# Kernel optimization log

Measured on AMD Instinct MI355X. Metric: run time of the kernel, lower is better.

The kernel has to match this reference:

```python
import jax, jax.numpy as jnp
import numpy as np

H = 1024       # hidden_size
R = 4          # downsacale_ratio -> bottleneck H//R = 256
DI = 2048      # mamba d_inner = expand * H
NS = 16        # d_state
KC = 4         # d_conv
DTR = 64       # dt_rank = ceil(H/16)
B, L = 4, 1024


def setup_inputs() -> dict:
    key = jax.random.key(0)
    ks = iter(jax.random.split(key, 32))
    w = lambda shape, s=0.02: jax.random.normal(next(ks), shape, jnp.float32) * s
    Hr = H // R
    inp = {
        'x': jax.random.normal(next(ks), (B, L, H), jnp.float32),
        't': jax.random.normal(next(ks), (B, H), jnp.float32),
        # adaLN modulation: SiLU -> Linear(H, 3H)
        'ada_w': w((H, 3 * H)), 'ada_b': jnp.zeros((3 * H,), jnp.float32),
        # hg_dense: Linear(H,H/R) SiLU Linear(H/R,H)
        'hgd_w1': w((H, Hr)), 'hgd_b1': jnp.zeros((Hr,), jnp.float32),
        'hgd_w2': w((Hr, H)), 'hgd_b2': jnp.zeros((H,), jnp.float32),
        # Mamba params
        'in_proj_w': w((H, 2 * DI)),
        'conv_w': w((DI, KC), 0.1), 'conv_b': jnp.zeros((DI,), jnp.float32),
        'x_proj_w': w((DI, DTR + 2 * NS)),
        'dt_proj_w': w((DTR, DI), 0.1),
        'dt_proj_b': jnp.log(jnp.expm1(jnp.full((DI,), 0.01, jnp.float32))),  # softplus^-1(0.01)
        'A_log': jnp.log(jnp.broadcast_to(jnp.arange(1, NS + 1, dtype=jnp.float32), (DI, NS))),
        'Dp': jnp.ones((DI,), jnp.float32),
        'out_proj_w': w((DI, H)),
        # hg_fuse
        'fm_w': w((H, Hr)), 'fm_b': jnp.zeros((Hr,), jnp.float32),
        'fr_w': w((H, Hr)), 'fr_b': jnp.zeros((Hr,), jnp.float32),
        'ff_w': w((Hr, H)), 'ff_b': jnp.zeros((H,), jnp.float32),
    }
    return inp


def _ln(x, eps=1e-6):
    mu = jnp.mean(x, -1, keepdims=True)
    var = jnp.mean(jnp.square(x - mu), -1, keepdims=True)
    return (x - mu) / jnp.sqrt(var + eps)


def _mamba(xd, in_proj_w, conv_w, conv_b, x_proj_w, dt_proj_w, dt_proj_b, A_log, Dp, out_proj_w):
    # xd: [B, L, H]
    xz = xd @ in_proj_w                      # [B, L, 2*DI]
    xm, z = jnp.split(xz, 2, axis=-1)
    # causal depthwise conv over time
    xc = jnp.swapaxes(xm, 1, 2)              # [B, DI, L]
    xc = jax.lax.conv_general_dilated(
        xc, conv_w[:, None, :], window_strides=(1,), padding=[(KC - 1, 0)],
        feature_group_count=DI, dimension_numbers=('NCH', 'OIH', 'NCH'))
    xc = jax.nn.silu(jnp.swapaxes(xc, 1, 2) + conv_b)   # [B, L, DI]
    dbl = xc @ x_proj_w                      # [B, L, DTR + 2*NS]
    dt = jax.nn.softplus(dbl[..., :DTR] @ dt_proj_w + dt_proj_b)   # [B, L, DI]
    Bm = dbl[..., DTR:DTR + NS]              # [B, L, NS]
    Cm = dbl[..., DTR + NS:]                 # [B, L, NS]
    A = -jnp.exp(A_log)                      # [DI, NS]

    def step(h, inp):
        dt_t, x_t, B_t, C_t = inp            # [B,DI],[B,DI],[B,NS],[B,NS]
        dA = jnp.exp(dt_t[:, :, None] * A)                       # [B, DI, NS]
        h = dA * h + (dt_t * x_t)[:, :, None] * B_t[:, None, :]
        y = jnp.einsum('bdn,bn->bd', h, C_t)
        return h, y

    h0 = jnp.zeros((xd.shape[0], DI, NS), xd.dtype)
    seq = (jnp.moveaxis(dt, 1, 0), jnp.moveaxis(xc, 1, 0),
           jnp.moveaxis(Bm, 1, 0), jnp.moveaxis(Cm, 1, 0))
    _, ys = jax.lax.scan(step, h0, seq)
    y = jnp.moveaxis(ys, 0, 1) + xc * Dp     # [B, L, DI]
    y = y * jax.nn.silu(z)
    return y @ out_proj_w                    # [B, L, H]


def reference(x, t, ada_w, ada_b, hgd_w1, hgd_b1, hgd_w2, hgd_b2,
              in_proj_w, conv_w, conv_b, x_proj_w, dt_proj_w, dt_proj_b,
              A_log, Dp, out_proj_w, fm_w, fm_b, fr_w, fr_b, ff_w, ff_b):
    ada = jax.nn.silu(t) @ ada_w + ada_b               # [B, 3H]
    shift, scale, alpha = jnp.split(ada, 3, axis=-1)
    x1 = _ln(x) * (1 + scale[:, None, :]) + shift[:, None, :]
    xd = jax.nn.silu(x1 @ hgd_w1 + hgd_b1) @ hgd_w2 + hgd_b2
    x1_2 = _mamba(xd, in_proj_w, conv_w, conv_b, x_proj_w, dt_proj_w,
                  dt_proj_b, A_log, Dp, out_proj_w)
    a = jax.nn.silu(x1_2 @ fm_w + fm_b)
    b = jax.nn.silu(x1 @ fr_w + fr_b)
    fuse = (a * b) @ ff_w + ff_b
    return x + alpha[:, None, :] * fuse
```

## Files before the change

### kernel.cpp

```cpp
#include <hip/hip_runtime.h>
#include <math.h>
#include <stdint.h>

#define H_   1024
#define HR_  256
#define DI_  2048
#define NS_  16
#define KC_  4
#define DTR_ 64
#define B_   4
#define L_   1024
#define ROWS (B_*L_)
#define H3_  3072
#define NCH_ 32
#define CL_  32
#define CLT_ 8

typedef short bf16x8 __attribute__((ext_vector_type(8)));
typedef float f32x4  __attribute__((ext_vector_type(4)));

#if __has_builtin(__builtin_amdgcn_exp2f)
#define EXP2(x) __builtin_amdgcn_exp2f(x)
#else
#define EXP2(x) __expf((x) * 0.6931471805599453f)
#endif
#define LOG2E 1.4426950408889634f

__device__ __forceinline__ float silu_f(float v) { return v / (1.f + __expf(-v)); }

__device__ __forceinline__ uint32_t pack_bf16_2(float a, float b) {
    uint32_t ua = __float_as_uint(a);
    uint32_t ub = __float_as_uint(b);
    uint32_t ra = (ua + 0x7FFFu + ((ua >> 16) & 1u)) >> 16;
    uint32_t rb = (ub + 0x7FFFu + ((ub >> 16) & 1u)) >> 16;
    return ra | (rb << 16);
}
__device__ __forceinline__ unsigned short cvt_bf16(float a) {
    uint32_t ua = __float_as_uint(a);
    return (unsigned short)((ua + 0x7FFFu + ((ua >> 16) & 1u)) >> 16);
}
__device__ __forceinline__ float bf16_to_f(unsigned short u) {
    return __uint_as_float(((uint32_t)u) << 16);
}

__device__ __forceinline__ void gload16(const short* g, short* l) {
    __builtin_amdgcn_global_load_lds(
        (const __attribute__((address_space(1))) void*)g,
        (__attribute__((address_space(3))) void*)l, 16, 0, 0);
}

#define TW_HGDFR 0ull
#define TW_HGD2  524288ull
#define TW_INPJ  786432ull
#define TW_XPJ   4980736ull
#define TW_DTPJ  5242880ull
#define TW_OPJ   5373952ull
#define TW_FM    7471104ull
#define TW_FF    7733248ull
#define TWT      7995392ull

__global__ __launch_bounds__(256) void wtrans_kernel(
    const float* __restrict__ s0, const float* __restrict__ s1,
    const float* __restrict__ s2, const float* __restrict__ s3,
    const float* __restrict__ s4, const float* __restrict__ s5,
    const float* __restrict__ s6, const float* __restrict__ s7,
    const float* __restrict__ s8, short* __restrict__ wt)
{
    int bid = blockIdx.x;
    const float* src; short* dst; int K, N, rel;
    if      (bid < 256)  { src = s0; dst = wt + TW_HGDFR;          K = 1024; N = 256;  rel = bid; }
    else if (bid < 512)  { src = s1; dst = wt + TW_HGDFR + 262144; K = 1024; N = 256;  rel = bid - 256; }
    else if (bid < 768)  { src = s2; dst = wt + TW_HGD2;           K = 256;  N = 1024; rel = bid - 512; }
    else if (bid < 4864) { src = s3; dst = wt + TW_INPJ;           K = 1024; N = 4096; rel = bid - 768; }
    else if (bid < 5120) { src = s4; dst = wt + TW_XPJ;            K = 2048; N = 96;   rel = bid - 4864; }
    else if (bid < 5248) { src = s5; dst = wt + TW_DTPJ;           K = 64;   N = 2048; rel = bid - 5120; }
    else if (bid < 7296) { src = s6; dst = wt + TW_OPJ;            K = 2048; N = 1024; rel = bid - 5248; }
    else if (bid < 7552) { src = s7; dst = wt + TW_FM;             K = 1024; N = 256;  rel = bid - 7296; }
    else                 { src = s8; dst = wt + TW_FF;             K = 256;  N = 1024; rel = bid - 7552; }
    int tkc = K >> 5;
    int tk = rel % tkc, tn = rel / tkc;

    __shared__ float ld[32][33];
    int tx = threadIdx.x & 7, ty = threadIdx.x >> 3;
    int kk = tk * 32 + ty, nn = tn * 32 + tx * 4;
    float4 v = make_float4(0.f, 0.f, 0.f, 0.f);
    if (nn < N) v = *(const float4*)&src[(size_t)kk * N + nn];
    ld[ty][tx * 4 + 0] = v.x; ld[ty][tx * 4 + 1] = v.y;
    ld[ty][tx * 4 + 2] = v.z; ld[ty][tx * 4 + 3] = v.w;
    __syncthreads();
    int nn2 = tn * 32 + ty, kk2 = tk * 32 + tx * 4;
    float a0 = ld[tx * 4 + 0][ty], a1 = ld[tx * 4 + 1][ty];
    float a2 = ld[tx * 4 + 2][ty], a3 = ld[tx * 4 + 3][ty];
    uint2 p = { pack_bf16_2(a0, a1), pack_bf16_2(a2, a3) };
    *(uint2*)&dst[(size_t)nn2 * K + kk2] = p;
}

__global__ __launch_bounds__(256) void cwt_kernel(
    const float* __restrict__ conv_w, float* __restrict__ cwt)
{
    int d = blockIdx.x * 256 + threadIdx.x;
    float4 v = *(const float4*)&conv_w[d * KC_];
    cwt[0 * DI_ + d] = v.x;
    cwt[1 * DI_ + d] = v.y;
    cwt[2 * DI_ + d] = v.z;
    cwt[3 * DI_ + d] = v.w;
}

__global__ __launch_bounds__(256) void ada_part_kernel(
    const float* __restrict__ t, const float* __restrict__ ada_w,
    float* __restrict__ part)
{
    int col = blockIdx.x * 1024 + threadIdx.x * 4;
    int b = blockIdx.y, z = blockIdx.z;
    __shared__ float st[32];
    if (threadIdx.x < 32) {
        float v = t[b * H_ + z * 32 + threadIdx.x];
        st[threadIdx.x] = silu_f(v);
    }
    __syncthreads();
    float4 acc = make_float4(0.f, 0.f, 0.f, 0.f);
    const float* w = ada_w + (size_t)(z * 32) * H3_ + col;
    #pragma unroll
    for (int k = 0; k < 32; ++k) {
        float4 wv = *(const float4*)(w + (size_t)k * H3_);
        float s = st[k];
        acc.x = fmaf(s, wv.x, acc.x);
        acc.y = fmaf(s, wv.y, acc.y);
        acc.z = fmaf(s, wv.z, acc.z);
        acc.w = fmaf(s, wv.w, acc.w);
    }
    *(float4*)&part[((size_t)z * B_ + b) * H3_ + col] = acc;
}

__global__ __launch_bounds__(256) void ada_red_kernel(
    const float* __restrict__ part, const float* __restrict__ ada_b,
    float* __restrict__ ada)
{
    int i = (blockIdx.x * 256 + threadIdx.x) * 4;
    int b = i / H3_, col = i - b * H3_;
    float4 s = make_float4(0.f, 0.f, 0.f, 0.f);
    #pragma unroll
    for (int z = 0; z < 32; ++z) {
        float4 p = *(const float4*)&part[((size_t)z * B_ + b) * H3_ + col];
        s.x += p.x; s.y += p.y; s.z += p.z; s.w += p.w;
    }
    float4 bv = *(const float4*)&ada_b[col];
    s.x += bv.x; s.y += bv.y; s.z += bv.z; s.w += bv.w;
    *(float4*)&ada[(size_t)b * H3_ + col] = s;
}

__global__ __launch_bounds__(256) void ln_mod_kernel(
    const float* __restrict__ x, const float* __restrict__ ada,
    short* __restrict__ x1b)
{
    int row = blockIdx.x;
    int b   = row >> 10;
    const float* xr = x + (size_t)row * H_;
    float4 v = ((const float4*)xr)[threadIdx.x];
    float s  = v.x + v.y + v.z + v.w;
    float s2 = v.x*v.x + v.y*v.y + v.z*v.z + v.w*v.w;

    __shared__ float red[8];
    int wave = threadIdx.x >> 6, lane = threadIdx.x & 63;
    #pragma unroll
    for (int off = 32; off; off >>= 1) {
        s  += __shfl_down(s,  off);
        s2 += __shfl_down(s2, off);
    }
    if (lane == 0) { red[wave] = s; red[4 + wave] = s2; }
    __syncthreads();
    float ts  = red[0] + red[1] + red[2] + red[3];
    float ts2 = red[4] + red[5] + red[6] + red[7];
    float mu  = ts  * (1.f / H_);
    float var = ts2 * (1.f / H_) - mu * mu;
    float inv = rsqrtf(var + 1e-6f);

    const float* sh = ada + b * H3_;
    int i = threadIdx.x * 4;
    float4 sh4 = *(const float4*)&sh[i];
    float4 sc4 = *(const float4*)&sh[H_ + i];
    float ox = (v.x - mu) * inv * (1.f + sc4.x) + sh4.x;
    float oy = (v.y - mu) * inv * (1.f + sc4.y) + sh4.y;
    float oz = (v.z - mu) * inv * (1.f + sc4.z) + sh4.z;
    float ow = (v.w - mu) * inv * (1.f + sc4.w) + sh4.w;
    uint2 p = { pack_bf16_2(ox, oy), pack_bf16_2(oz, ow) };
    *(uint2*)(x1b + (size_t)row * H_ + i) = p;
}

template<int ACT, bool SPLITK>
__global__ __launch_bounds__(256) void gemm128(
    const short* __restrict__ A, int lda,
    const short* __restrict__ Wt, int ldw,
    const float* __restrict__ bias,
    float* __restrict__ C, short* __restrict__ Cb, short* __restrict__ Cb2,
    int ldc, int M, int N, int K,
    const float* __restrict__ E0, const float* __restrict__ E1)
{
    __shared__ short As[3][4096];
    __shared__ short Bs[3][4096];
    int tid  = threadIdx.x;
    int lane = tid & 63, wv = tid >> 6, wm = wv >> 1, wn = wv & 1;
    int n0 = blockIdx.x * 128;
    int m0 = blockIdx.y * 128;

    if (SPLITK) {
        int z = blockIdx.z;
        A  += (size_t)z * K;
        Wt += (size_t)z * K;
        C  += (size_t)z * M * N;
    }

    int r = lane & 15, g = lane >> 4;
    int sA = wv * 2;
    const short* ga0 = A  + (size_t)(m0 + sA * 16 + r) * lda + g * 8;
    const short* ga1 = ga0 + (size_t)16 * lda;
    const short* gb0 = Wt + (size_t)(n0 + sA * 16 + r) * ldw + g * 8;
    const short* gb1 = gb0 + (size_t)16 * ldw;

    f32x4 acc[4][4];
    #pragma unroll
    for (int i = 0; i < 4; ++i)
        #pragma unroll
        for (int j = 0; j < 4; ++j) {
            acc[i][j][0] = 0.f; acc[i][j][1] = 0.f;
            acc[i][j][2] = 0.f; acc[i][j][3] = 0.f;
        }

    #define STAGE(buf, koff)                                    \
        do {                                                    \
            gload16(ga0 + (koff), &As[buf][sA * 512]);          \
            gload16(ga1 + (koff), &As[buf][sA * 512 + 512]);    \
            gload16(gb0 + (koff), &Bs[buf][sA * 512]);          \
            gload16(gb1 + (koff), &Bs[buf][sA * 512 + 512]);    \
        } while (0)

    #define COMPUTE(buf)                                                          \
        do {                                                                      \
            bf16x8 af[4], bfr[4];                                                 \
            _Pragma("unroll")                                                     \
            for (int i = 0; i < 4; ++i)                                           \
                af[i] = *(const bf16x8*)&As[buf][(wm * 4 + i) * 512 + lane * 8];  \
            _Pragma("unroll")                                                     \
            for (int j = 0; j < 4; ++j)                                           \
                bfr[j] = *(const bf16x8*)&Bs[buf][(wn * 4 + j) * 512 + lane * 8]; \
            _Pragma("unroll")                                                     \
            for (int i = 0; i < 4; ++i)                                           \
                _Pragma("unroll")                                                 \
                for (int j = 0; j < 4; ++j)                                       \
                    acc[i][j] = __builtin_amdgcn_mfma_f32_16x16x32_bf16(          \
                        af[i], bfr[j], acc[i][j], 0, 0, 0);                       \
        } while (0)

    int T = K >> 5;
    STAGE(0, 0);
    if (T > 1) STAGE(1, 32);
    for (int t = 0; t < T; ++t) {
        if (t + 1 < T) asm volatile("s_waitcnt vmcnt(4)" ::: "memory");
        else           asm volatile("s_waitcnt vmcnt(0)" ::: "memory");
        __builtin_amdgcn_s_barrier();
        if (t + 2 < T) STAGE((t + 2) % 3, (t + 2) * 32);
        COMPUTE(t % 3);
    }
    #undef STAGE
    #undef COMPUTE

    #pragma unroll
    for (int i = 0; i < 4; ++i) {
        int mb = m0 + wm * 64 + i * 16 + ((lane >> 4) << 2);
        #pragma unroll
        for (int j = 0; j < 4; ++j) {
            int n = n0 + wn * 64 + j * 16 + (lane & 15);
            if (n < N) {
                float bv;
                if (ACT == 6) bv = (n < 256) ? bias[n] : E0[n - 256];
                else          bv = bias ? bias[n] : 0.f;
                #pragma unroll
                for (int rr = 0; rr < 4; ++rr) {
                    int m = mb + rr;
                    float v = acc[i][j][rr] + bv;
                    size_t ci = (size_t)m * ldc + n;
                    if (ACT == 6) {
                        float sv = silu_f(v);
                        if (n < 256) Cb[(size_t)m * 256 + n]        = (short)cvt_bf16(sv);
                        else         Cb2[(size_t)m * 256 + (n-256)] = (short)cvt_bf16(sv);
                    } else {
                        if (ACT == 2) v = (v > 20.f) ? v : log1pf(__expf(v));
                        else if (ACT == 4) {
                            int bb = m >> 10;
                            v = E0[ci] + E1[bb * H3_ + 2 * H_ + n] * v;
                        }
                        if (C)  C[ci]  = v;
                        if (Cb) Cb[ci] = (short)cvt_bf16(v);
                    }
                }
            }
        }
    }
}

template<int ACT>
__global__ __launch_bounds__(512) void gemm256(
    const short* __restrict__ A, int lda,
    const short* __restrict__ Wt, int ldw,
    short* __restrict__ Cb, int M, int N, int K)
{
    extern __shared__ short lds[];
    short* Asb = lds;
    short* Bsb = lds + 24576;
    int tid  = threadIdx.x;
    int lane = tid & 63, wv = tid >> 6;
    int wm = wv >> 2, wn = wv & 3;
    int n0 = blockIdx.x * 256;
    int m0 = blockIdx.y * 256;

    int r = lane & 15, g = lane >> 4;
    int sA = wv * 2;
    const short* ga0 = A  + (size_t)(m0 + sA * 16 + r) * lda + g * 8;
    const short* ga1 = ga0 + (size_t)16 * lda;
    const short* gb0 = Wt + (size_t)(n0 + sA * 16 + r) * ldw + g * 8;
    const short* gb1 = gb0 + (size_t)16 * ldw;

    f32x4 acc[8][4];
    #pragma unroll
    for (int i = 0; i < 8; ++i)
        #pragma unroll
        for (int j = 0; j < 4; ++j) {
            acc[i][j][0] = 0.f; acc[i][j][1] = 0.f;
            acc[i][j][2] = 0.f; acc[i][j][3] = 0.f;
        }

    #define STAGE2(buf, koff)                                       \
        do {                                                        \
            gload16(ga0 + (koff), &Asb[(buf) * 8192 + sA * 512]);   \
            gload16(ga1 + (koff), &Asb[(buf) * 8192 + sA * 512 + 512]); \
            gload16(gb0 + (koff), &Bsb[(buf) * 8192 + sA * 512]);   \
            gload16(gb1 + (koff), &Bsb[(buf) * 8192 + sA * 512 + 512]); \
        } while (0)

    int T = K >> 5;
    STAGE2(0, 0);
    if (T > 1) STAGE2(1, 32);
    for (int t = 0; t < T; ++t) {
        if (t + 1 < T) asm volatile("s_waitcnt vmcnt(4)" ::: "memory");
        else           asm volatile("s_waitcnt vmcnt(0)" ::: "memory");
        __builtin_amdgcn_s_barrier();
        if (t + 2 < T) STAGE2((t + 2) % 3, (t + 2) * 32);
        {
            int buf = t % 3;
            bf16x8 af[8], bfr[4];
            #pragma unroll
            for (int i = 0; i < 8; ++i)
                af[i] = *(const bf16x8*)&Asb[buf * 8192 + (wm * 8 + i) * 512 + lane * 8];
            #pragma unroll
            for (int j = 0; j < 4; ++j)
                bfr[j] = *(const bf16x8*)&Bsb[buf * 8192 + (wn * 4 + j) * 512 + lane * 8];
            __builtin_amdgcn_s_setprio(1);
            #pragma unroll
            for (int i = 0; i < 8; ++i)
                #pragma unroll
                for (int j = 0; j < 4; ++j)
                    acc[i][j] = __builtin_amdgcn_mfma_f32_16x16x32_bf16(
                        af[i], bfr[j], acc[i][j], 0, 0, 0);
            __builtin_amdgcn_s_setprio(0);
        }
    }
    #undef STAGE2

    #pragma unroll
    for (int i = 0; i < 8; ++i) {
        int mb = m0 + wm * 128 + i * 16 + ((lane >> 4) << 2);
        #pragma unroll
        for (int j = 0; j < 4; ++j) {
            int n = n0 + wn * 64 + j * 16 + (lane & 15);
            #pragma unroll
            for (int rr = 0; rr < 4; ++rr) {
                int m = mb + rr;
                float v = acc[i][j][rr];
                if (ACT == 5) {
                    size_t idx = (n < DI_) ? ((size_t)m * DI_ + n)
                                           : ((size_t)ROWS * DI_ + (size_t)m * DI_ + (n - DI_));
                    Cb[idx] = (short)cvt_bf16(v);
                }
            }
        }
    }
}

template<int ACT, bool SPLITK>
__global__ __launch_bounds__(512) void gemm256d(
    const short* __restrict__ A, int lda,
    const short* __restrict__ Wt, int ldw,
    short* __restrict__ Cb, int ldc,
    int M, int N, int K)
{
    extern __shared__ short lds[];
    short* Asb = lds;
    short* Bsb = lds + 16384;
    int tid  = threadIdx.x;
    int lane = tid & 63, wv = tid >> 6;
    int wm = wv >> 2, wn = wv & 3;
    int n0 = blockIdx.x * 256;
    int m0 = blockIdx.y * 256;

    if (SPLITK) {
        int z = blockIdx.z;
        A  += (size_t)z * K;
        Wt += (size_t)z * K;
        Cb += (size_t)z * M * N;
    }

    int r = lane & 15, g = lane >> 4;
    int sA = wv * 2;
    const short* ga0 = A  + (size_t)(m0 + sA * 16 + r) * lda + g * 8;
    const short* ga1 = ga0 + (size_t)16 * lda;
    const short* gb0 = Wt + (size_t)(n0 + sA * 16 + r) * ldw + g * 8;
    const short* gb1 = gb0 + (size_t)16 * ldw;

    f32x4 acc[8][4];
    #pragma unroll
    for (int i = 0; i < 8; ++i)
        #pragma unroll
        for (int j = 0; j < 4; ++j) {
            acc[i][j][0] = 0.f; acc[i][j][1] = 0.f;
            acc[i][j][2] = 0.f; acc[i][j][3] = 0.f;
        }

    #define STAGE2(buf, koff)                                       \
        do {                                                        \
            gload16(ga0 + (koff), &Asb[(buf) * 8192 + sA * 512]);   \
            gload16(ga1 + (koff), &Asb[(buf) * 8192 + sA * 512 + 512]); \
            gload16(gb0 + (koff), &Bsb[(buf) * 8192 + sA * 512]);   \
            gload16(gb1 + (koff), &Bsb[(buf) * 8192 + sA * 512 + 512]); \
        } while (0)

    int T = K >> 5;
    STAGE2(0, 0);
    __syncthreads();
    int cur = 0;
    for (int t = 0; t < T; ++t) {
        if (t + 1 < T) STAGE2(cur ^ 1, (t + 1) * 32);
        {
            bf16x8 af[8], bfr[4];
            #pragma unroll
            for (int i = 0; i < 8; ++i)
                af[i] = *(const bf16x8*)&Asb[cur * 8192 + (wm * 8 + i) * 512 + lane * 8];
            #pragma unroll
            for (int j = 0; j < 4; ++j)
                bfr[j] = *(const bf16x8*)&Bsb[cur * 8192 + (wn * 4 + j) * 512 + lane * 8];
            __builtin_amdgcn_s_setprio(1);
            #pragma unroll
            for (int i = 0; i < 8; ++i)
                #pragma unroll
                for (int j = 0; j < 4; ++j)
                    acc[i][j] = __builtin_amdgcn_mfma_f32_16x16x32_bf16(
                        af[i], bfr[j], acc[i][j], 0, 0, 0);
            __builtin_amdgcn_s_setprio(0);
        }
        __syncthreads();
        cur ^= 1;
    }
    #undef STAGE2

    #pragma unroll
    for (int i = 0; i < 8; ++i) {
        int mb = m0 + wm * 128 + i * 16 + ((lane >> 4) << 2);
        #pragma unroll
        for (int j = 0; j < 4; ++j) {
            int n = n0 + wn * 64 + j * 16 + (lane & 15);
            #pragma unroll
            for (int rr = 0; rr < 4; ++rr) {
                int m = mb + rr;
                float v = acc[i][j][rr];
                if (ACT == 8) {
                    Cb[(size_t)m * ldc + n] = (short)cvt_bf16(v);
                }
            }
        }
    }
}

__global__ __launch_bounds__(256) void redk_xproj(
    const float* __restrict__ part, float* __restrict__ dbl,
    short* __restrict__ dblb)
{
    size_t i = ((size_t)blockIdx.x * 256 + threadIdx.x) * 4;
    const size_t seg = (size_t)ROWS * 96;
    float4 s = *(const float4*)(part + i);
    #pragma unroll
    for (int z = 1; z < 8; ++z) {
        float4 p = *(const float4*)(part + z * seg + i);
        s.x += p.x; s.y += p.y; s.z += p.z; s.w += p.w;
    }
    *(float4*)(dbl + i) = s;
    uint2 p = { pack_bf16_2(s.x, s.y), pack_bf16_2(s.z, s.w) };
    *(uint2*)(dblb + i) = p;
}

__global__ __launch_bounds__(256) void redk_hgdfr(
    const float* __restrict__ part, const float* __restrict__ hgd_b1,
    const float* __restrict__ fr_b, short* __restrict__ h1b,
    short* __restrict__ frlin)
{
    size_t i = ((size_t)blockIdx.x * 256 + threadIdx.x) * 4;
    const size_t seg = (size_t)ROWS * 512;
    int m   = (int)(i >> 9);
    int col = (int)(i & 511);
    float4 a = *(const float4*)(part + i);
    float4 b = *(const float4*)(part + seg + i);
    float s0 = a.x + b.x, s1 = a.y + b.y, s2 = a.z + b.z, s3 = a.w + b.w;
    const float* bias = (col < 256) ? (hgd_b1 + col) : (fr_b + col - 256);
    float4 bv = *(const float4*)bias;
    float o0 = silu_f(s0 + bv.x), o1 = silu_f(s1 + bv.y);
    float o2 = silu_f(s2 + bv.z), o3 = silu_f(s3 + bv.w);
    uint2 p = { pack_bf16_2(o0, o1), pack_bf16_2(o2, o3) };
    short* dst = (col < 256) ? (h1b + (size_t)m * 256 + col)
                             : (frlin + (size_t)m * 256 + col - 256);
    *(uint2*)dst = p;
}

__global__ __launch_bounds__(256) void redk_op4(
    const short* __restrict__ part, short* __restrict__ x12b)
{
    size_t i = ((size_t)blockIdx.x * 256 + threadIdx.x) * 8;
    const size_t seg = (size_t)ROWS * H_;
    float s[8];
    bf16x8 p0 = *(const bf16x8*)(part + i);
    #pragma unroll
    for (int e = 0; e < 8; ++e) s[e] = bf16_to_f((unsigned short)p0[e]);
    #pragma unroll
    for (int z = 1; z < 4; ++z) {
        bf16x8 pz = *(const bf16x8*)(part + z * seg + i);
        #pragma unroll
        for (int e = 0; e < 8; ++e) s[e] += bf16_to_f((unsigned short)pz[e]);
    }
    bf16x8 o;
    #pragma unroll
    for (int e = 0; e < 8; ++e) o[e] = (short)cvt_bf16(s[e]);
    *(bf16x8*)(x12b + i) = o;
}

__global__ __launch_bounds__(256) void redk_fm(
    const float* __restrict__ part, const float* __restrict__ fm_b,
    const short* __restrict__ frlin, short* __restrict__ abb)
{
    size_t i = ((size_t)blockIdx.x * 256 + threadIdx.x) * 4;
    const size_t seg = (size_t)ROWS * HR_;
    float4 s = *(const float4*)(part + i);
    #pragma unroll
    for (int z = 1; z < 4; ++z) {
        float4 p = *(const float4*)(part + z * seg + i);
        s.x += p.x; s.y += p.y; s.z += p.z; s.w += p.w;
    }
    int col = (int)(i & (HR_ - 1));
    float4 b = *(const float4*)(fm_b + col);
    const short* fr = frlin + i;
    float o0 = silu_f(s.x + b.x) * bf16_to_f((unsigned short)fr[0]);
    float o1 = silu_f(s.y + b.y) * bf16_to_f((unsigned short)fr[1]);
    float o2 = silu_f(s.z + b.z) * bf16_to_f((unsigned short)fr[2]);
    float o3 = silu_f(s.w + b.w) * bf16_to_f((unsigned short)fr[3]);
    uint2 p = { pack_bf16_2(o0, o1), pack_bf16_2(o2, o3) };
    *(uint2*)(abb + i) = p;
}

__global__ __launch_bounds__(256) void conv_kernel(
    const short* __restrict__ xmb, const float* __restrict__ cwt,
    const float* __restrict__ conv_b, short* __restrict__ xcb)
{
    int d0 = threadIdx.x * 8;
    int b  = blockIdx.y;
    int l0 = blockIdx.x * CLT_;

    float w[KC_][8];
    #pragma unroll
    for (int j = 0; j < KC_; ++j) {
        float4 a = *(const float4*)&cwt[j * DI_ + d0];
        float4 c = *(const float4*)&cwt[j * DI_ + d0 + 4];
        w[j][0] = a.x; w[j][1] = a.y; w[j][2] = a.z; w[j][3] = a.w;
        w[j][4] = c.x; w[j][5] = c.y; w[j][6] = c.z; w[j][7] = c.w;
    }
    float bia[8];
    {
        float4 b0 = *(const float4*)&conv_b[d0];
        float4 b1 = *(const float4*)&conv_b[d0 + 4];
        bia[0] = b0.x; bia[1] = b0.y; bia[2] = b0.z; bia[3] = b0.w;
        bia[4] = b1.x; bia[5] = b1.y; bia[6] = b1.z; bia[7] = b1.w;
    }

    const short* base = xmb + (size_t)b * L_ * DI_ + d0;
    short*       outb = xcb + (size_t)b * L_ * DI_ + d0;

    bf16x8 win[KC_];
    #pragma unroll
    for (int j = 0; j < KC_ - 1; ++j) {
        int ll = l0 - (KC_ - 1) + j;
        if (ll >= 0) win[j] = *(const bf16x8*)(base + (size_t)ll * DI_);
        else         win[j] = (bf16x8)0;
    }
    for (int l = l0; l < l0 + CLT_; ++l) {
        win[KC_ - 1] = *(const bf16x8*)(base + (size_t)l * DI_);
        bf16x8 o;
        #pragma unroll
        for (int e = 0; e < 8; ++e) {
            float acc = bia[e];
            #pragma unroll
            for (int j = 0; j < KC_; ++j)
                acc = fmaf(bf16_to_f((unsigned short)win[j][e]), w[j][e], acc);
            o[e] = (short)cvt_bf16(silu_f(acc));
        }
        *(bf16x8*)(outb + (size_t)l * DI_) = o;
        win[0] = win[1]; win[1] = win[2]; win[2] = win[3];
    }
}

__global__ __launch_bounds__(256) void scan_part1(
    const short* __restrict__ dtb, const short* __restrict__ xcb,
    const float* __restrict__ dbl, const float* __restrict__ A_log,
    float* __restrict__ hend, float* __restrict__ dtsum)
{
    int bx = blockIdx.x;
    int dg = bx & 15;
    int bc = bx >> 4;
    int c  = bc & (NCH_ - 1);
    int b  = bc >> 5;
    int tid  = threadIdx.x;
    int lane = tid & 63, wv = tid >> 6;
    int dl   = tid >> 1;
    int d    = dg * 128 + dl;
    int half = tid & 1;
    int n0   = half * 8;

    __shared__ float sB[CL_][NS_];
    __shared__ short dtS[2][16][128];
    __shared__ short xcS[2][16][128];

    size_t srcoff = (size_t)(b * L_ + c * CL_ + wv * 4 + (lane >> 4)) * DI_
                    + dg * 128 + (lane & 15) * 8;
    const short* gdt = dtb + srcoff;
    const short* gxc = xcb + srcoff;

    #define SSTG1(buf, q)                                             \
        do {                                                          \
            gload16(gdt + (size_t)(q) * 16 * DI_, &dtS[buf][wv*4][0]); \
            gload16(gxc + (size_t)(q) * 16 * DI_, &xcS[buf][wv*4][0]); \
        } while (0)

    SSTG1(0, 0);
    for (int idx = tid; idx < CL_ * NS_; idx += 256) {
        int l = idx >> 4, n = idx & 15;
        sB[l][n] = dbl[(size_t)(b * L_ + c * CL_ + l) * 96 + DTR_ + n];
    }
    float Aa2[8];
    #pragma unroll
    for (int n = 0; n < 8; ++n)
        Aa2[n] = -__expf(A_log[d * NS_ + n0 + n]) * LOG2E;

    float h[8];
    #pragma unroll
    for (int n = 0; n < 8; ++n) h[n] = 0.f;
    float sdt = 0.f;

    __syncthreads();
    int buf = 0;
    for (int q = 0; q < 2; ++q) {
        if (q < 1) SSTG1(buf ^ 1, q + 1);
        #pragma unroll
        for (int li = 0; li < 16; ++li) {
            int l = q * 16 + li;
            float dtv = bf16_to_f((unsigned short)dtS[buf][li][dl]);
            float xv  = bf16_to_f((unsigned short)xcS[buf][li][dl]);
            float du  = dtv * xv;
            sdt += dtv;
            #pragma unroll
            for (int n = 0; n < 8; ++n)
                h[n] = fmaf(EXP2(dtv * Aa2[n]), h[n], du * sB[l][n0 + n]);
        }
        __syncthreads();
        buf ^= 1;
    }
    #undef SSTG1

    #pragma unroll
    for (int n = 0; n < 8; ++n)
        hend[((size_t)((b * NCH_ + c) * NS_ + n0 + n)) * DI_ + d] = h[n];
    if (half == 0)
        dtsum[(size_t)(b * NCH_ + c) * DI_ + d] = sdt;
}

__global__ __launch_bounds__(256) void scan_mid(
    const float* __restrict__ hend, const float* __restrict__ dtsum,
    const float* __restrict__ A_log, float* __restrict__ hin)
{
    int idx = blockIdx.x * 256 + threadIdx.x;
    int d  = idx & (DI_ - 1);
    int bn = idx >> 11;
    int n  = bn & (NS_ - 1);
    int b  = bn >> 4;
    float Aa2 = -__expf(A_log[d * NS_ + n]) * LOG2E;
    float h = 0.f;
    #pragma unroll
    for (int c = 0; c < NCH_; ++c) {
        size_t o = ((size_t)((b * NCH_ + c) * NS_ + n)) * DI_ + d;
        hin[o] = h;
        float s = dtsum[(size_t)(b * NCH_ + c) * DI_ + d];
        h = fmaf(EXP2(Aa2 * s), h, hend[o]);
    }
}

__global__ __launch_bounds__(256) void scan_part2(
    const short* __restrict__ dtb, const short* __restrict__ xcb,
    const short* __restrict__ zb, const float* __restrict__ dbl,
    const float* __restrict__ A_log, const float* __restrict__ Dp,
    const float* __restrict__ hin, short* __restrict__ y2b)
{
    int bx = blockIdx.x;
    int dg = bx & 15;
    int bc = bx >> 4;
    int c  = bc & (NCH_ - 1);
    int b  = bc >> 5;
    int tid  = threadIdx.x;
    int lane = tid & 63, wv = tid >> 6;
    int dl   = tid >> 1;
    int d    = dg * 128 + dl;
    int half = tid & 1;
    int n0   = half * 8;

    __shared__ float sBC[CL_][2 * NS_];
    __shared__ short dtS[2][16][128];
    __shared__ short xcS[2][16][128];
    __shared__ short zS[2][16][128];

    size_t srcoff = (size_t)(b * L_ + c * CL_ + wv * 4 + (lane >> 4)) * DI_
                    + dg * 128 + (lane & 15) * 8;
    const short* gdt = dtb + srcoff;
    const short* gxc = xcb + srcoff;
    const short* gz  = zb  + srcoff;

    #define SSTG2(buf, q)                                             \
        do {                                                          \
            gload16(gdt + (size_t)(q) * 16 * DI_, &dtS[buf][wv*4][0]); \
            gload16(gxc + (size_t)(q) * 16 * DI_, &xcS[buf][wv*4][0]); \
            gload16(gz  + (size_t)(q) * 16 * DI_, &zS[buf][wv*4][0]);  \
        } while (0)

    SSTG2(0, 0);
    for (int idx = tid; idx < CL_ * 2 * NS_; idx += 256) {
        int l = idx >> 5, n = idx & 31;
        sBC[l][n] = dbl[(size_t)(b * L_ + c * CL_ + l) * 96 + DTR_ + n];
    }
    float Aa2[8];
    #pragma unroll
    for (int n = 0; n < 8; ++n)
        Aa2[n] = -__expf(A_log[d * NS_ + n0 + n]) * LOG2E;

    float h[8];
    #pragma unroll
    for (int n = 0; n < 8; ++n)
        h[n] = hin[((size_t)((b * NCH_ + c) * NS_ + n0 + n)) * DI_ + d];
    float Dpv = Dp[d];
    size_t obase = (size_t)(b * L_ + c * CL_) * DI_ + d;

    __syncthreads();
    int buf = 0;
    for (int q = 0; q < 2; ++q) {
        if (q < 1) SSTG2(buf ^ 1, q + 1);
        #pragma unroll
        for (int li = 0; li < 16; ++li) {
            int l = q * 16 + li;
            float dtv = bf16_to_f((unsigned short)dtS[buf][li][dl]);
            float xv  = bf16_to_f((unsigned short)xcS[buf][li][dl]);
            float zv  = bf16_to_f((unsigned short)zS[buf][li][dl]);
            float du  = dtv * xv;
            float y = 0.f;
            #pragma unroll
            for (int n = 0; n < 8; ++n) {
                float dA = EXP2(dtv * Aa2[n]);
                h[n] = fmaf(dA, h[n], du * sBC[l][n0 + n]);
                y = fmaf(h[n], sBC[l][NS_ + n0 + n], y);
            }
            y += __shfl_xor(y, 1);
            if (half == 0) {
                y = fmaf(xv, Dpv, y);
                y2b[obase + (size_t)l * DI_] = (short)cvt_bf16(y * silu_f(zv));
            }
        }
        __syncthreads();
        buf ^= 1;
    }
    #undef SSTG2
}

extern "C" void kernel_launch(void* const* d_in, const int* in_sizes, int n_in,
                              void* d_out, int out_size, void* d_ws, size_t ws_size,
                              hipStream_t stream)
{
    const float* x         = (const float*)d_in[0];
    const float* t         = (const float*)d_in[1];
    const float* ada_w     = (const float*)d_in[2];
    const float* ada_b     = (const float*)d_in[3];
    const float* hgd_w1    = (const float*)d_in[4];
    const float* hgd_b1    = (const float*)d_in[5];
    const float* hgd_w2    = (const float*)d_in[6];
    const float* hgd_b2    = (const float*)d_in[7];
    const float* in_proj_w = (const float*)d_in[8];
    const float* conv_w    = (const float*)d_in[9];
    const float* conv_b    = (const float*)d_in[10];
    const float* x_proj_w  = (const float*)d_in[11];
    const float* dt_proj_w = (const float*)d_in[12];
    const float* dt_proj_b = (const float*)d_in[13];
    const float* A_log     = (const float*)d_in[14];
    const float* Dp        = (const float*)d_in[15];
    const float* out_proj_w= (const float*)d_in[16];
    const float* fm_w      = (const float*)d_in[17];
    const float* fm_b      = (const float*)d_in[18];
    const float* fr_w      = (const float*)d_in[19];
    const float* fr_b      = (const float*)d_in[20];
    const float* ff_w      = (const float*)d_in[21];
    const float* ff_b      = (const float*)d_in[22];
    float* out = (float*)d_out;

    char* p = (char*)d_ws;
    auto alloc = [&](size_t bytes) { char* r = p; p += (bytes + 255) & ~255ull; return r; };

    short* wt      = (short*)alloc(TWT * 2);
    float* cwt     = (float*)alloc((size_t)KC_ * DI_ * 4);
    short* x1b     = (short*)alloc((size_t)ROWS * H_ * 2);
    short* h1b     = (short*)alloc((size_t)ROWS * HR_ * 2);
    short* frlin   = (short*)alloc((size_t)ROWS * HR_ * 2);
    short* xdb     = (short*)alloc((size_t)ROWS * H_ * 2);
    short* xmzb    = (short*)alloc((size_t)ROWS * DI_ * 4);
    short* xcb     = (short*)alloc((size_t)ROWS * DI_ * 2);
    short* y2b     = (short*)alloc((size_t)ROWS * DI_ * 2);
    short* dtb     = (short*)alloc((size_t)ROWS * DI_ * 2);
    float* scratch = (float*)alloc((size_t)4 * ROWS * H_ * 4);
    float* dbl     = (float*)alloc((size_t)ROWS * 96 * 4);
    short* dblb    = (short*)alloc((size_t)ROWS * 96 * 2);
    short* x12b    = (short*)alloc((size_t)ROWS * H_ * 2);
    short* abb     = (short*)alloc((size_t)ROWS * HR_ * 2);
    float* ada     = (float*)alloc((size_t)B_ * H3_ * 4);

    short* xmb   = xmzb;
    short* zb    = xmzb + (size_t)ROWS * DI_;
    float* dtsum = (float*)abb;
    float* adapart = scratch;
    float* hfpart  = scratch;
    float* xppart  = scratch;
    float* hend    = scratch;
    float* hin     = scratch + (size_t)B_ * NCH_ * NS_ * DI_;
    short* oppart  = (short*)scratch;
    float* fmpart  = scratch;

    dim3 blk(256), b512(512);

    wtrans_kernel<<<dim3(7808), blk, 0, stream>>>(
        hgd_w1, fr_w, hgd_w2, in_proj_w, x_proj_w, dt_proj_w, out_proj_w,
        fm_w, ff_w, wt);
    cwt_kernel<<<dim3(DI_ / 256), blk, 0, stream>>>(conv_w, cwt);
    ada_part_kernel<<<dim3(3, B_, 32), blk, 0, stream>>>(t, ada_w, adapart);
    ada_red_kernel<<<dim3(B_ * H3_ / 4 / 256), blk, 0, stream>>>(adapart, ada_b, ada);
    ln_mod_kernel<<<dim3(ROWS), blk, 0, stream>>>(x, ada, x1b);
    gemm128<0, true><<<dim3(4, 32, 2), blk, 0, stream>>>(
        x1b, H_, wt + TW_HGDFR, H_, nullptr, hfpart, nullptr, nullptr,
        512, ROWS, 512, 512, nullptr, nullptr);
    redk_hgdfr<<<dim3(ROWS * 512 / 4 / 256), blk, 0, stream>>>(
        hfpart, hgd_b1, fr_b, h1b, frlin);
    gemm128<0, false><<<dim3(8, 32), blk, 0, stream>>>(
        h1b, HR_, wt + TW_HGD2, HR_, hgd_b2, nullptr, xdb, nullptr,
        H_, ROWS, H_, HR_, nullptr, nullptr);
    gemm256<5><<<dim3(16, 16), b512, 98304, stream>>>(
        xdb, H_, wt + TW_INPJ, H_, xmb, ROWS, 2 * DI_, H_);
    conv_kernel<<<dim3(L_ / CLT_, B_), blk, 0, stream>>>(xmb, cwt, conv_b, xcb);
    gemm128<0, true><<<dim3(1, 32, 8), blk, 0, stream>>>(
        xcb, DI_, wt + TW_XPJ, DI_, nullptr, xppart, nullptr, nullptr,
        96, ROWS, 96, 256, nullptr, nullptr);
    redk_xproj<<<dim3(ROWS * 96 / 4 / 256), blk, 0, stream>>>(xppart, dbl, dblb);
    gemm128<2, false><<<dim3(16, 32), blk, 0, stream>>>(
        dblb, 96, wt + TW_DTPJ, DTR_, dt_proj_b, nullptr, dtb, nullptr,
        DI_, ROWS, DI_, DTR_, nullptr, nullptr);
    scan_part1<<<dim3(B_ * NCH_ * 16), blk, 0, stream>>>(
        dtb, xcb, dbl, A_log, hend, dtsum);
    scan_mid<<<dim3(B_ * DI_ * NS_ / 256), blk, 0, stream>>>(
        hend, dtsum, A_log, hin);
    scan_part2<<<dim3(B_ * NCH_ * 16), blk, 0, stream>>>(
        dtb, xcb, zb, dbl, A_log, Dp, hin, y2b);
    gemm256d<8, true><<<dim3(4, 16, 4), b512, 65536, stream>>>(
        y2b, DI_, wt + TW_OPJ, DI_, oppart, H_, ROWS, H_, 512);
    redk_op4<<<dim3(ROWS * H_ / 8 / 256), blk, 0, stream>>>(oppart, x12b);
    gemm128<0, true><<<dim3(2, 32, 4), blk, 0, stream>>>(
        x12b, H_, wt + TW_FM, H_, nullptr, fmpart, nullptr, nullptr,
        HR_, ROWS, HR_, 256, nullptr, nullptr);
    redk_fm<<<dim3(ROWS * HR_ / 4 / 256), blk, 0, stream>>>(fmpart, fm_b, frlin, abb);
    gemm128<4, false><<<dim3(8, 32), blk, 0, stream>>>(
        abb, HR_, wt + TW_FF, HR_, ff_b, out, nullptr, nullptr,
        H_, ROWS, H_, HR_, x, ada);
}
```

Measured before the change: 334.1 us.

## Retile out_proj GEMM to 256x128 with triple-buffered LDS, unbuffer scan staging

The split-K out_proj GEMM moves from 256x256 to 256x128 tiles, which doubles the grid to 512 blocks. It also switches from double to triple-buffered LDS with explicit vmcnt waits and a single barrier per k-step, so global loads run two stages ahead and there are more blocks to fill the CUs. The scan kernels drop their double-buffered LDS staging and instead load the second half-chunk synchronously between two barriers. That reduces LDS use, likely to raise occupancy, but exposes load latency in the middle of the scan.

```diff
diff --git a/kernel.cpp b/kernel.cpp
--- a/kernel.cpp
+++ b/kernel.cpp
@@ -387,7 +387,7 @@
 }
 
 template<int ACT, bool SPLITK>
-__global__ __launch_bounds__(512) void gemm256d(
+__global__ __launch_bounds__(512) void gemm256x128(
     const short* __restrict__ A, int lda,
     const short* __restrict__ Wt, int ldw,
     short* __restrict__ Cb, int ldc,
@@ -395,11 +395,11 @@
 {
     extern __shared__ short lds[];
     short* Asb = lds;
-    short* Bsb = lds + 16384;
+    short* Bsb = lds + 24576;
     int tid  = threadIdx.x;
     int lane = tid & 63, wv = tid >> 6;
-    int wm = wv >> 2, wn = wv & 3;
-    int n0 = blockIdx.x * 256;
+    int wm = wv >> 1, wn = wv & 1;
+    int n0 = blockIdx.x * 128;
     int m0 = blockIdx.y * 256;
 
     if (SPLITK) {
@@ -413,57 +413,56 @@
     int sA = wv * 2;
     const short* ga0 = A  + (size_t)(m0 + sA * 16 + r) * lda + g * 8;
     const short* ga1 = ga0 + (size_t)16 * lda;
-    const short* gb0 = Wt + (size_t)(n0 + sA * 16 + r) * ldw + g * 8;
-    const short* gb1 = gb0 + (size_t)16 * ldw;
-
-    f32x4 acc[8][4];
-    #pragma unroll
-    for (int i = 0; i < 8; ++i)
+    const short* gb0 = Wt + (size_t)(n0 + wv * 16 + r) * ldw + g * 8;
+
+    f32x4 acc[4][4];
+    #pragma unroll
+    for (int i = 0; i < 4; ++i)
         #pragma unroll
         for (int j = 0; j < 4; ++j) {
             acc[i][j][0] = 0.f; acc[i][j][1] = 0.f;
             acc[i][j][2] = 0.f; acc[i][j][3] = 0.f;
         }
 
-    #define STAGE2(buf, koff)                                       \
+    #define STAGE3(buf, koff)                                       \
         do {                                                        \
             gload16(ga0 + (koff), &Asb[(buf) * 8192 + sA * 512]);   \
             gload16(ga1 + (koff), &Asb[(buf) * 8192 + sA * 512 + 512]); \
-            gload16(gb0 + (koff), &Bsb[(buf) * 8192 + sA * 512]);   \
-            gload16(gb1 + (koff), &Bsb[(buf) * 8192 + sA * 512 + 512]); \
+            gload16(gb0 + (koff), &Bsb[(buf) * 4096 + wv * 512]);   \
         } while (0)
 
     int T = K >> 5;
-    STAGE2(0, 0);
-    __syncthreads();
-    int cur = 0;
+    STAGE3(0, 0);
+    if (T > 1) STAGE3(1, 32);
     for (int t = 0; t < T; ++t) {
-        if (t + 1 < T) STAGE2(cur ^ 1, (t + 1) * 32);
+        if (t + 1 < T) asm volatile("s_waitcnt vmcnt(3)" ::: "memory");
+        else           asm volatile("s_waitcnt vmcnt(0)" ::: "memory");
+        __builtin_amdgcn_s_barrier();
+        if (t + 2 < T) STAGE3((t + 2) % 3, (t + 2) * 32);
         {
-            bf16x8 af[8], bfr[4];
-            #pragma unroll
-            for (int i = 0; i < 8; ++i)
-                af[i] = *(const bf16x8*)&Asb[cur * 8192 + (wm * 8 + i) * 512 + lane * 8];
+            int buf = t % 3;
+            bf16x8 af[4], bfr[4];
+            #pragma unroll
+            for (int i = 0; i < 4; ++i)
+                af[i] = *(const bf16x8*)&Asb[buf * 8192 + (wm * 4 + i) * 512 + lane * 8];
             #pragma unroll
             for (int j = 0; j < 4; ++j)
-                bfr[j] = *(const bf16x8*)&Bsb[cur * 8192 + (wn * 4 + j) * 512 + lane * 8];
+                bfr[j] = *(const bf16x8*)&Bsb[buf * 4096 + (wn * 4 + j) * 512 + lane * 8];
             __builtin_amdgcn_s_setprio(1);
             #pragma unroll
-            for (int i = 0; i < 8; ++i)
+            for (int i = 0; i < 4; ++i)
                 #pragma unroll
                 for (int j = 0; j < 4; ++j)
                     acc[i][j] = __builtin_amdgcn_mfma_f32_16x16x32_bf16(
                         af[i], bfr[j], acc[i][j], 0, 0, 0);
             __builtin_amdgcn_s_setprio(0);
         }
-        __syncthreads();
-        cur ^= 1;
-    }
-    #undef STAGE2
-
-    #pragma unroll
-    for (int i = 0; i < 8; ++i) {
-        int mb = m0 + wm * 128 + i * 16 + ((lane >> 4) << 2);
+    }
+    #undef STAGE3
+
+    #pragma unroll
+    for (int i = 0; i < 4; ++i) {
+        int mb = m0 + wm * 64 + i * 16 + ((lane >> 4) << 2);
         #pragma unroll
         for (int j = 0; j < 4; ++j) {
             int n = n0 + wn * 64 + j * 16 + (lane & 15);
@@ -630,21 +629,21 @@
     int n0   = half * 8;
 
     __shared__ float sB[CL_][NS_];
-    __shared__ short dtS[2][16][128];
-    __shared__ short xcS[2][16][128];
+    __shared__ short dtS[16][128];
+    __shared__ short xcS[16][128];
 
     size_t srcoff = (size_t)(b * L_ + c * CL_ + wv * 4 + (lane >> 4)) * DI_
                     + dg * 128 + (lane & 15) * 8;
     const short* gdt = dtb + srcoff;
     const short* gxc = xcb + srcoff;
 
-    #define SSTG1(buf, q)                                             \
+    #define SSTG1(q)                                                  \
         do {                                                          \
-            gload16(gdt + (size_t)(q) * 16 * DI_, &dtS[buf][wv*4][0]); \
-            gload16(gxc + (size_t)(q) * 16 * DI_, &xcS[buf][wv*4][0]); \
+            gload16(gdt + (size_t)(q) * 16 * DI_, &dtS[wv*4][0]);     \
+            gload16(gxc + (size_t)(q) * 16 * DI_, &xcS[wv*4][0]);     \
         } while (0)
 
-    SSTG1(0, 0);
+    SSTG1(0);
     for (int idx = tid; idx < CL_ * NS_; idx += 256) {
         int l = idx >> 4, n = idx & 15;
         sB[l][n] = dbl[(size_t)(b * L_ + c * CL_ + l) * 96 + DTR_ + n];
@@ -660,22 +659,23 @@
     float sdt = 0.f;
 
     __syncthreads();
-    int buf = 0;
     for (int q = 0; q < 2; ++q) {
-        if (q < 1) SSTG1(buf ^ 1, q + 1);
         #pragma unroll
         for (int li = 0; li < 16; ++li) {
             int l = q * 16 + li;
-            float dtv = bf16_to_f((unsigned short)dtS[buf][li][dl]);
-            float xv  = bf16_to_f((unsigned short)xcS[buf][li][dl]);
+            float dtv = bf16_to_f((unsigned short)dtS[li][dl]);
+            float xv  = bf16_to_f((unsigned short)xcS[li][dl]);
             float du  = dtv * xv;
             sdt += dtv;
             #pragma unroll
             for (int n = 0; n < 8; ++n)
                 h[n] = fmaf(EXP2(dtv * Aa2[n]), h[n], du * sB[l][n0 + n]);
         }
-        __syncthreads();
-        buf ^= 1;
+        if (q == 0) {
+            __syncthreads();
+            SSTG1(1);
+            __syncthreads();
+        }
     }
     #undef SSTG1
 
@@ -725,9 +725,9 @@
     int n0   = half * 8;
 
     __shared__ float sBC[CL_][2 * NS_];
-    __shared__ short dtS[2][16][128];
-    __shared__ short xcS[2][16][128];
-    __shared__ short zS[2][16][128];
+    __shared__ short dtS[16][128];
+    __shared__ short xcS[16][128];
+    __shared__ short zS[16][128];
 
     size_t srcoff = (size_t)(b * L_ + c * CL_ + wv * 4 + (lane >> 4)) * DI_
                     + dg * 128 + (lane & 15) * 8;
@@ -735,14 +735,14 @@
     const short* gxc = xcb + srcoff;
     const short* gz  = zb  + srcoff;
 
-    #define SSTG2(buf, q)                                             \
+    #define SSTG2(q)                                                  \
         do {                                                          \
-            gload16(gdt + (size_t)(q) * 16 * DI_, &dtS[buf][wv*4][0]); \
-            gload16(gxc + (size_t)(q) * 16 * DI_, &xcS[buf][wv*4][0]); \
-            gload16(gz  + (size_t)(q) * 16 * DI_, &zS[buf][wv*4][0]);  \
+            gload16(gdt + (size_t)(q) * 16 * DI_, &dtS[wv*4][0]);     \
+            gload16(gxc + (size_t)(q) * 16 * DI_, &xcS[wv*4][0]);     \
+            gload16(gz  + (size_t)(q) * 16 * DI_, &zS[wv*4][0]);      \
         } while (0)
 
-    SSTG2(0, 0);
+    SSTG2(0);
     for (int idx = tid; idx < CL_ * 2 * NS_; idx += 256) {
         int l = idx >> 5, n = idx & 31;
         sBC[l][n] = dbl[(size_t)(b * L_ + c * CL_ + l) * 96 + DTR_ + n];
@@ -760,15 +760,13 @@
     size_t obase = (size_t)(b * L_ + c * CL_) * DI_ + d;
 
     __syncthreads();
-    int buf = 0;
     for (int q = 0; q < 2; ++q) {
-        if (q < 1) SSTG2(buf ^ 1, q + 1);
         #pragma unroll
         for (int li = 0; li < 16; ++li) {
             int l = q * 16 + li;
-            float dtv = bf16_to_f((unsigned short)dtS[buf][li][dl]);
-            float xv  = bf16_to_f((unsigned short)xcS[buf][li][dl]);
-            float zv  = bf16_to_f((unsigned short)zS[buf][li][dl]);
+            float dtv = bf16_to_f((unsigned short)dtS[li][dl]);
+            float xv  = bf16_to_f((unsigned short)xcS[li][dl]);
+            float zv  = bf16_to_f((unsigned short)zS[li][dl]);
             float du  = dtv * xv;
             float y = 0.f;
             #pragma unroll
@@ -783,8 +781,11 @@
                 y2b[obase + (size_t)l * DI_] = (short)cvt_bf16(y * silu_f(zv));
             }
         }
-        __syncthreads();
-        buf ^= 1;
+        if (q == 0) {
+            __syncthreads();
+            SSTG2(1);
+            __syncthreads();
+        }
     }
     #undef SSTG2
 }
@@ -882,7 +883,7 @@
         hend, dtsum, A_log, hin);
     scan_part2<<<dim3(B_ * NCH_ * 16), blk, 0, stream>>>(
         dtb, xcb, zb, dbl, A_log, Dp, hin, y2b);
-    gemm256d<8, true><<<dim3(4, 16, 4), b512, 65536, stream>>>(
+    gemm256x128<8, true><<<dim3(8, 16, 4), b512, 73728, stream>>>(
         y2b, DI_, wt + TW_OPJ, DI_, oppart, H_, ROWS, H_, 512);
     redk_op4<<<dim3(ROWS * H_ / 8 / 256), blk, 0, stream>>>(oppart, x12b);
     gemm128<0, true><<<dim3(2, 32, 4), blk, 0, stream>>>(
```

Measured after the change: 338.9 us. About the same (+1.4%).
